# Kernel optimization log

Measured on AMD Instinct MI355X. Metric: run time of the kernel, lower is better.

## Reference

```python
import jax, jax.numpy as jnp
import numpy as np

UNITS = 64
CHANNEL = 64
L1 = 32
L2 = 32
BATCH = 64


def setup_inputs() -> dict:
    key = jax.random.key(0)
    k1, k2, k3, k4, k5 = jax.random.split(key, 5)
    input_dim = CHANNEL + 3 * UNITS
    inputs = jax.random.normal(k1, (BATCH, CHANNEL, L1, L2), dtype=jnp.float32)
    W = jax.random.normal(k2, (input_dim, UNITS * 7), dtype=jnp.float32) * (1.0 / np.sqrt(input_dim))
    U_rec = jax.random.normal(k3, (UNITS * 3, UNITS), dtype=jnp.float32) * (1.0 / np.sqrt(UNITS * 3))
    bias = jnp.zeros((UNITS * 8,), dtype=jnp.float32)
    W_ij = jax.random.normal(k4, (CHANNEL, UNITS), dtype=jnp.float32) * (1.0 / np.sqrt(CHANNEL))
    return {"inputs": inputs, "W": W, "U_rec": U_rec, "bias": bias, "W_ij": W_ij}


def reference(inputs, W, U_rec, bias, W_ij):
    B, C, l1, l2 = inputs.shape
    u = W_ij.shape[1]
    wr, br = W[:, : 3 * u], bias[: 3 * u]
    wz, bz = W[:, 3 * u : 7 * u], bias[3 * u : 7 * u]
    b_ij = bias[7 * u :]

    # [L1*L2, B, C] scan order: row-major over (i, j), direction 'lt'
    x = jnp.transpose(inputs, (2, 3, 0, 1)).reshape(l1 * l2, B, C)
    states0 = jnp.zeros((l1 + 1, l2 + 1, B, u), dtype=inputs.dtype)  # zero boundary

    def step(carry, xs):
        states, _ = carry
        s_ij, t = xs
        i = t // l2
        j = t % l2
        h_diag = states[i, j]        # [B, u]
        h_top = states[i, j + 1]
        h_left = states[i + 1, j]
        # q = [h_top, h_left, h_diag, s_ij] : [B, 3u + C]
        q = jnp.concatenate([h_top, h_left, h_diag, s_ij], axis=1)
        r = jax.nn.sigmoid(q @ wr + br)                     # [B, 3u]
        z = q @ wz + bz                                     # [B, 4u]
        zg = jax.nn.softmax(z.reshape(B, 4, u), axis=1)     # softmax across 4 gates per unit
        zi, zl, zt, zd = zg[:, 0], zg[:, 1], zg[:, 2], zg[:, 3]
        h_hat = jnp.tanh(
            s_ij @ W_ij + b_ij
            + (r * jnp.concatenate([h_left, h_top, h_diag], axis=1)) @ U_rec
        )
        h_ij = zl * h_left + zt * h_top + zd * h_diag + zi * h_hat
        states = states.at[i + 1, j + 1].set(h_ij)
        return (states, h_ij), None

    tsteps = jnp.arange(l1 * l2)
    (_, h_last), _ = jax.lax.scan(
        step, (states0, jnp.zeros((B, u), dtype=inputs.dtype)), (x, tsteps)
    )
    return h_last
```

## Files before the change

### kernel.cpp

```cpp
#include <hip/hip_runtime.h>
#include <cstdint>
#include <cstddef>


#define LDIM   32
#define BATCH  64
#define UNITS  64
#define CHAN   64
#define NBT    4
#define BT     16
#define TPB    512

typedef _Float16 f16;
typedef _Float16 f16x8 __attribute__((ext_vector_type(8)));
typedef float    f32x4 __attribute__((ext_vector_type(4)));

__global__ __launch_bounds__(TPB, 2) void spatial_gru_kernel(
    const float* __restrict__ x,
    const float* __restrict__ W,
    const float* __restrict__ Urec,
    const float* __restrict__ bias,
    const float* __restrict__ Wij,
    float* __restrict__ out,
    uint32_t* __restrict__ hbuf)
{
    const int bid = blockIdx.x;
    const int row = bid >> 2;
    const int bt  = bid & 3;
    const int b0  = bt * BT;
    const int t   = (int)threadIdx.x;
    const int u   = t & 63;
    const int g   = t >> 6;
    const int l15 = t & 15;
    const int lq  = (t & 63) >> 4;

    __shared__ __attribute__((aligned(16))) f16 qf[BT][264];
    __shared__ __attribute__((aligned(16))) f16 rf[BT][200];
    __shared__ float qs32[BT][204];
    __shared__ float Gsz [BT][260];
    __shared__ float pacc[4][BT][68];

    f16x8 wreg[4][8];
    float bias1[4] = {0.f, 0.f, 0.f, 0.f};
    if (g < 7) {
        const int nb = g * 64 + l15;
#pragma unroll
        for (int T = 0; T < 4; ++T) {
            bias1[T] = bias[nb + 16 * T];
#pragma unroll
            for (int s = 0; s < 8; ++s) {
                f16x8 v;
#pragma unroll
                for (int jj = 0; jj < 8; ++jj) {
                    int kk = s * 32 + lq * 8 + jj;
                    v[jj] = (f16)W[(size_t)kk * 448 + nb + 16 * T];
                }
                wreg[T][s] = v;
            }
        }
    }
    f16x8 wreg2[4][2];
    {
        const int kb = (g & 3) * 64;
#pragma unroll
        for (int T = 0; T < 4; ++T) {
            const int nn = T * 16 + l15;
#pragma unroll
            for (int s = 0; s < 2; ++s) {
                f16x8 v;
#pragma unroll
                for (int jj = 0; jj < 8; ++jj) {
                    int kk = kb + s * 32 + lq * 8 + jj;
                    float wv = (kk < 192) ? Urec[kk * 64 + nn] : Wij[(kk - 192) * 64 + nn];
                    v[jj] = (f16)wv;
                }
                wreg2[T][s] = v;
            }
        }
    }
    const float bij = bias[448 + u];

    for (int idx = t; idx < 192 * BT; idx += TPB) {
        int b = idx & 15, k = idx >> 4;
        qs32[b][k] = 0.f;
        qf[b][k] = (f16)0.f;
    }

    const size_t xb0 = (size_t)(b0 + g) * 65536 + (size_t)u * 1024 + (size_t)row * 32;
    const size_t xb1 = xb0 + (size_t)8 * 65536;
    {
        float x0 = x[xb0], x1 = x[xb1];
        qf[g][192 + u]     = (f16)x0;
        qf[g + 8][192 + u] = (f16)x1;
    }
    __syncthreads();

    for (int j = 0; j < LDIM; ++j) {
        float ht0 = 0.f, ht1 = 0.f;
        f16 hf0 = (f16)0.f, hf1 = (f16)0.f;
        if (row > 0) {
            const uint32_t* sp =
                hbuf + ((((size_t)(row - 1) * LDIM + j) * NBT + bt) << 9) + (g << 6) + u;
            uint32_t w = __hip_atomic_load(sp, __ATOMIC_RELAXED, __HIP_MEMORY_SCOPE_AGENT);
            while ((w & 0x00010001u) != 0x00010001u) {
                __builtin_amdgcn_s_sleep(1);
                w = __hip_atomic_load(sp, __ATOMIC_RELAXED, __HIP_MEMORY_SCOPE_AGENT);
            }
            uint16_t lo = (uint16_t)(w & 0xFFFFu), hi = (uint16_t)(w >> 16);
            hf0 = __builtin_bit_cast(f16, lo);
            hf1 = __builtin_bit_cast(f16, hi);
            ht0 = (float)hf0;
            ht1 = (float)hf1;
        }
        qs32[g][u]     = ht0;  qf[g][u]     = hf0;
        qs32[g + 8][u] = ht1;  qf[g + 8][u] = hf1;
        __syncthreads();

        float nx0 = 0.f, nx1 = 0.f;
        if (j < LDIM - 1) { nx0 = x[xb0 + j + 1]; nx1 = x[xb1 + j + 1]; }

        if (g < 7) {
            f32x4 acc[4];
#pragma unroll
            for (int T = 0; T < 4; ++T)
                acc[T] = (f32x4){bias1[T], bias1[T], bias1[T], bias1[T]};
#pragma unroll
            for (int s = 0; s < 8; ++s) {
                f16x8 a = *(const f16x8*)&qf[l15][s * 32 + lq * 8];
#pragma unroll
                for (int T = 0; T < 4; ++T)
                    acc[T] = __builtin_amdgcn_mfma_f32_16x16x32_f16(a, wreg[T][s], acc[T], 0, 0, 0);
            }
            if (g < 3) {
                const int colbase = (g == 0) ? 64 : (g == 1) ? 0 : 128;
#pragma unroll
                for (int T = 0; T < 4; ++T)
#pragma unroll
                    for (int r = 0; r < 4; ++r) {
                        float rr = 1.f / (1.f + __expf(-acc[T][r]));
                        int b = lq * 4 + r;
                        float hv = qs32[b][colbase + T * 16 + l15];
                        rf[b][g * 64 + T * 16 + l15] = (f16)(rr * hv);
                    }
            } else {
                const int zb = (g - 3) * 64;
#pragma unroll
                for (int T = 0; T < 4; ++T)
#pragma unroll
                    for (int r = 0; r < 4; ++r)
                        Gsz[lq * 4 + r][zb + T * 16 + l15] = acc[T][r];
            }
        } else {
            f32x4 a2[4];
#pragma unroll
            for (int T = 0; T < 4; ++T) a2[T] = (f32x4){0.f, 0.f, 0.f, 0.f};
#pragma unroll
            for (int s = 0; s < 2; ++s) {
                f16x8 a = *(const f16x8*)&qf[l15][192 + s * 32 + lq * 8];
#pragma unroll
                for (int T = 0; T < 4; ++T)
                    a2[T] = __builtin_amdgcn_mfma_f32_16x16x32_f16(a, wreg2[T][s], a2[T], 0, 0, 0);
            }
#pragma unroll
            for (int T = 0; T < 4; ++T)
#pragma unroll
                for (int r = 0; r < 4; ++r)
                    pacc[3][lq * 4 + r][T * 16 + l15] = a2[T][r];
        }
        __syncthreads();

        if (g >= 4 && g < 7) {
            const int w  = g - 4;
            const int kb = w * 64;
            f32x4 a2[4];
#pragma unroll
            for (int T = 0; T < 4; ++T) a2[T] = (f32x4){0.f, 0.f, 0.f, 0.f};
#pragma unroll
            for (int s = 0; s < 2; ++s) {
                f16x8 a = *(const f16x8*)&rf[l15][kb + s * 32 + lq * 8];
#pragma unroll
                for (int T = 0; T < 4; ++T)
                    a2[T] = __builtin_amdgcn_mfma_f32_16x16x32_f16(a, wreg2[T][s], a2[T], 0, 0, 0);
            }
#pragma unroll
            for (int T = 0; T < 4; ++T)
#pragma unroll
                for (int r = 0; r < 4; ++r)
                    pacc[w][lq * 4 + r][T * 16 + l15] = a2[T][r];
        }
        __syncthreads();

        float hvv[2], hTv[2];
#pragma unroll
        for (int i = 0; i < 2; ++i) {
            int b = g + 8 * i;
            float hhv = bij + pacc[0][b][u] + pacc[1][b][u] + pacc[2][b][u] + pacc[3][b][u];
            float e2 = __expf(2.f * hhv);
            float th = 1.f - 2.f / (e2 + 1.f);
            float zi = Gsz[b][u],       zl = Gsz[b][64 + u];
            float zt = Gsz[b][128 + u], zd = Gsz[b][192 + u];
            float mx = fmaxf(fmaxf(zi, zl), fmaxf(zt, zd));
            float ei = __expf(zi - mx), el = __expf(zl - mx);
            float et = __expf(zt - mx), ed = __expf(zd - mx);
            float inv = 1.f / (ei + el + et + ed);
            float hT = qs32[b][u], hL = qs32[b][64 + u], hD = qs32[b][128 + u];
            float hv = (el * hL + et * hT + ed * hD + ei * th) * inv;
            hvv[i] = hv; hTv[i] = hT;
        }
        {
            uint16_t lo = (uint16_t)(__builtin_bit_cast(uint16_t, (f16)hvv[0]) | 1u);
            uint16_t hi = (uint16_t)(__builtin_bit_cast(uint16_t, (f16)hvv[1]) | 1u);
            uint32_t pw = ((uint32_t)hi << 16) | lo;
            __hip_atomic_store(
                hbuf + ((((size_t)row * LDIM + j) * NBT + bt) << 9) + (g << 6) + u,
                pw, __ATOMIC_RELAXED, __HIP_MEMORY_SCOPE_AGENT);
        }
        if (row == LDIM - 1 && j == LDIM - 1) {
            out[(size_t)(b0 + g) * UNITS + u]     = hvv[0];
            out[(size_t)(b0 + g + 8) * UNITS + u] = hvv[1];
        }
#pragma unroll
        for (int i = 0; i < 2; ++i) {
            int b = g + 8 * i;
            qs32[b][128 + u] = hTv[i];
            qs32[b][64 + u]  = hvv[i];
            f16 htf = qf[b][u];
            qf[b][128 + u] = htf;
            qf[b][64 + u]  = (f16)hvv[i];
        }
        qf[g][192 + u]     = (f16)nx0;
        qf[g + 8][192 + u] = (f16)nx1;
    }
}

extern "C" void kernel_launch(void* const* d_in, const int* in_sizes, int n_in,
                              void* d_out, int out_size, void* d_ws, size_t ws_size,
                              hipStream_t stream) {
    const float* x    = (const float*)d_in[0];
    const float* W    = (const float*)d_in[1];
    const float* Urec = (const float*)d_in[2];
    const float* bias = (const float*)d_in[3];
    const float* Wij  = (const float*)d_in[4];
    float* out = (float*)d_out;

    uint32_t* hbuf = (uint32_t*)d_ws;

    spatial_gru_kernel<<<LDIM * NBT, TPB, 0, stream>>>(
        x, W, Urec, bias, Wij, out, hbuf);
}
```

Baseline: 264.8 us.

## Overlap cross-block h_top wait with local MFMAs and restructure the gate epilogue

After: 358.4 us. 35.3% more time.

```diff
diff --git a/kernel.cpp b/kernel.cpp
--- a/kernel.cpp
+++ b/kernel.cpp
@@ -14,6 +14,7 @@
 typedef _Float16 f16;
 typedef _Float16 f16x8 __attribute__((ext_vector_type(8)));
 typedef float    f32x4 __attribute__((ext_vector_type(4)));
+typedef uint32_t u32x4 __attribute__((ext_vector_type(4)));
 
 __global__ __launch_bounds__(TPB, 2) void spatial_gru_kernel(
     const float* __restrict__ x,
@@ -60,7 +61,7 @@
         }
     }
     f16x8 wreg2[4][2];
-    {
+    if (g >= 4) {
         const int kb = (g & 3) * 64;
 #pragma unroll
         for (int T = 0; T < 4; ++T) {
@@ -80,8 +81,8 @@
     }
     const float bij = bias[448 + u];
 
-    for (int idx = t; idx < 192 * BT; idx += TPB) {
-        int b = idx & 15, k = idx >> 4;
+    for (int idx = t; idx < 128 * BT; idx += TPB) {
+        int b = idx & 15, k = 64 + (idx >> 4);
         qs32[b][k] = 0.f;
         qf[b][k] = (f16)0.f;
     }
@@ -93,54 +94,90 @@
         qf[g][192 + u]     = (f16)x0;
         qf[g + 8][192 + u] = (f16)x1;
     }
-    __syncthreads();
 
     for (int j = 0; j < LDIM; ++j) {
-        float ht0 = 0.f, ht1 = 0.f;
-        f16 hf0 = (f16)0.f, hf1 = (f16)0.f;
+        __syncthreads();
+
+        uint32_t d0=0,d1=0,d2=0,d3=0,d4=0,d5=0,d6=0,d7=0;
+        const uint32_t* sp = hbuf;
         if (row > 0) {
-            const uint32_t* sp =
-                hbuf + ((((size_t)(row - 1) * LDIM + j) * NBT + bt) << 9) + (g << 6) + u;
-            uint32_t w = __hip_atomic_load(sp, __ATOMIC_RELAXED, __HIP_MEMORY_SCOPE_AGENT);
-            while ((w & 0x00010001u) != 0x00010001u) {
-                __builtin_amdgcn_s_sleep(1);
-                w = __hip_atomic_load(sp, __ATOMIC_RELAXED, __HIP_MEMORY_SCOPE_AGENT);
-            }
-            uint16_t lo = (uint16_t)(w & 0xFFFFu), hi = (uint16_t)(w >> 16);
-            hf0 = __builtin_bit_cast(f16, lo);
-            hf1 = __builtin_bit_cast(f16, hi);
-            ht0 = (float)hf0;
-            ht1 = (float)hf1;
-        }
-        qs32[g][u]     = ht0;  qf[g][u]     = hf0;
-        qs32[g + 8][u] = ht1;  qf[g + 8][u] = hf1;
-        __syncthreads();
-
+            sp = hbuf + ((((size_t)(row - 1) * LDIM + j) * NBT + bt) << 9)
+                      + (l15 * 32 + lq * 4);
+            d0 = __hip_atomic_load(sp + 0,  __ATOMIC_RELAXED, __HIP_MEMORY_SCOPE_AGENT);
+            d1 = __hip_atomic_load(sp + 1,  __ATOMIC_RELAXED, __HIP_MEMORY_SCOPE_AGENT);
+            d2 = __hip_atomic_load(sp + 2,  __ATOMIC_RELAXED, __HIP_MEMORY_SCOPE_AGENT);
+            d3 = __hip_atomic_load(sp + 3,  __ATOMIC_RELAXED, __HIP_MEMORY_SCOPE_AGENT);
+            d4 = __hip_atomic_load(sp + 16, __ATOMIC_RELAXED, __HIP_MEMORY_SCOPE_AGENT);
+            d5 = __hip_atomic_load(sp + 17, __ATOMIC_RELAXED, __HIP_MEMORY_SCOPE_AGENT);
+            d6 = __hip_atomic_load(sp + 18, __ATOMIC_RELAXED, __HIP_MEMORY_SCOPE_AGENT);
+            d7 = __hip_atomic_load(sp + 19, __ATOMIC_RELAXED, __HIP_MEMORY_SCOPE_AGENT);
+        }
         float nx0 = 0.f, nx1 = 0.f;
         if (j < LDIM - 1) { nx0 = x[xb0 + j + 1]; nx1 = x[xb1 + j + 1]; }
 
+        f32x4 acc[4];
         if (g < 7) {
-            f32x4 acc[4];
 #pragma unroll
             for (int T = 0; T < 4; ++T)
                 acc[T] = (f32x4){bias1[T], bias1[T], bias1[T], bias1[T]};
 #pragma unroll
-            for (int s = 0; s < 8; ++s) {
+            for (int s = 2; s < 8; ++s) {
                 f16x8 a = *(const f16x8*)&qf[l15][s * 32 + lq * 8];
 #pragma unroll
                 for (int T = 0; T < 4; ++T)
                     acc[T] = __builtin_amdgcn_mfma_f32_16x16x32_f16(a, wreg[T][s], acc[T], 0, 0, 0);
             }
+        } else {
+            f32x4 a2[4];
+#pragma unroll
+            for (int T = 0; T < 4; ++T) a2[T] = (f32x4){0.f, 0.f, 0.f, 0.f};
+#pragma unroll
+            for (int s = 0; s < 2; ++s) {
+                f16x8 a = *(const f16x8*)&qf[l15][192 + s * 32 + lq * 8];
+#pragma unroll
+                for (int T = 0; T < 4; ++T)
+                    a2[T] = __builtin_amdgcn_mfma_f32_16x16x32_f16(a, wreg2[T][s], a2[T], 0, 0, 0);
+            }
+#pragma unroll
+            for (int T = 0; T < 4; ++T)
+#pragma unroll
+                for (int r = 0; r < 4; ++r)
+                    pacc[3][lq * 4 + r][T * 16 + l15] = a2[T][r];
+        }
+
+        f16x8 ha0, ha1;
+#pragma unroll
+        for (int jj = 0; jj < 8; ++jj) { ha0[jj] = (f16)0.f; ha1[jj] = (f16)0.f; }
+        if (row > 0) {
+            while (((d0 & d1 & d2 & d3 & d4 & d5 & d6 & d7) & 0x00010001u) != 0x00010001u) {
+                __builtin_amdgcn_s_sleep(1);
+                d0 = __hip_atomic_load(sp + 0,  __ATOMIC_RELAXED, __HIP_MEMORY_SCOPE_AGENT);
+                d1 = __hip_atomic_load(sp + 1,  __ATOMIC_RELAXED, __HIP_MEMORY_SCOPE_AGENT);
+                d2 = __hip_atomic_load(sp + 2,  __ATOMIC_RELAXED, __HIP_MEMORY_SCOPE_AGENT);
+                d3 = __hip_atomic_load(sp + 3,  __ATOMIC_RELAXED, __HIP_MEMORY_SCOPE_AGENT);
+                d4 = __hip_atomic_load(sp + 16, __ATOMIC_RELAXED, __HIP_MEMORY_SCOPE_AGENT);
+                d5 = __hip_atomic_load(sp + 17, __ATOMIC_RELAXED, __HIP_MEMORY_SCOPE_AGENT);
+                d6 = __hip_atomic_load(sp + 18, __ATOMIC_RELAXED, __HIP_MEMORY_SCOPE_AGENT);
+                d7 = __hip_atomic_load(sp + 19, __ATOMIC_RELAXED, __HIP_MEMORY_SCOPE_AGENT);
+            }
+            ha0 = __builtin_bit_cast(f16x8, (u32x4){d0, d1, d2, d3});
+            ha1 = __builtin_bit_cast(f16x8, (u32x4){d4, d5, d6, d7});
+        }
+
+        if (g < 7) {
+#pragma unroll
+            for (int T = 0; T < 4; ++T)
+                acc[T] = __builtin_amdgcn_mfma_f32_16x16x32_f16(ha0, wreg[T][0], acc[T], 0, 0, 0);
+#pragma unroll
+            for (int T = 0; T < 4; ++T)
+                acc[T] = __builtin_amdgcn_mfma_f32_16x16x32_f16(ha1, wreg[T][1], acc[T], 0, 0, 0);
             if (g < 3) {
-                const int colbase = (g == 0) ? 64 : (g == 1) ? 0 : 128;
 #pragma unroll
                 for (int T = 0; T < 4; ++T)
 #pragma unroll
                     for (int r = 0; r < 4; ++r) {
                         float rr = 1.f / (1.f + __expf(-acc[T][r]));
-                        int b = lq * 4 + r;
-                        float hv = qs32[b][colbase + T * 16 + l15];
-                        rf[b][g * 64 + T * 16 + l15] = (f16)(rr * hv);
+                        rf[lq * 4 + r][g * 64 + T * 16 + l15] = (f16)rr;
                     }
             } else {
                 const int zb = (g - 3) * 64;
@@ -151,33 +188,29 @@
                         Gsz[lq * 4 + r][zb + T * 16 + l15] = acc[T][r];
             }
         } else {
-            f32x4 a2[4];
-#pragma unroll
-            for (int T = 0; T < 4; ++T) a2[T] = (f32x4){0.f, 0.f, 0.f, 0.f};
-#pragma unroll
-            for (int s = 0; s < 2; ++s) {
-                f16x8 a = *(const f16x8*)&qf[l15][192 + s * 32 + lq * 8];
-#pragma unroll
-                for (int T = 0; T < 4; ++T)
-                    a2[T] = __builtin_amdgcn_mfma_f32_16x16x32_f16(a, wreg2[T][s], a2[T], 0, 0, 0);
-            }
-#pragma unroll
-            for (int T = 0; T < 4; ++T)
-#pragma unroll
-                for (int r = 0; r < 4; ++r)
-                    pacc[3][lq * 4 + r][T * 16 + l15] = a2[T][r];
+#pragma unroll
+            for (int jj = 0; jj < 8; ++jj) {
+                qs32[l15][lq * 8 + jj]      = (float)ha0[jj];
+                qs32[l15][32 + lq * 8 + jj] = (float)ha1[jj];
+            }
         }
         __syncthreads();
 
         if (g >= 4 && g < 7) {
             const int w  = g - 4;
             const int kb = w * 64;
+            const int hb = (w == 0) ? 64 : (w == 1) ? 0 : 128;
             f32x4 a2[4];
 #pragma unroll
             for (int T = 0; T < 4; ++T) a2[T] = (f32x4){0.f, 0.f, 0.f, 0.f};
 #pragma unroll
             for (int s = 0; s < 2; ++s) {
-                f16x8 a = *(const f16x8*)&rf[l15][kb + s * 32 + lq * 8];
+                f16x8 a;
+#pragma unroll
+                for (int jj = 0; jj < 8; ++jj) {
+                    int kk = s * 32 + lq * 8 + jj;
+                    a[jj] = (f16)((float)rf[l15][kb + kk] * qs32[l15][hb + kk]);
+                }
 #pragma unroll
                 for (int T = 0; T < 4; ++T)
                     a2[T] = __builtin_amdgcn_mfma_f32_16x16x32_f16(a, wreg2[T][s], a2[T], 0, 0, 0);
@@ -187,33 +220,39 @@
 #pragma unroll
                 for (int r = 0; r < 4; ++r)
                     pacc[w][lq * 4 + r][T * 16 + l15] = a2[T][r];
+        } else if (g < 4) {
+#pragma unroll
+            for (int i = 0; i < 4; ++i) {
+                const int b = g * 4 + i;
+                float zi = Gsz[b][u],       zl = Gsz[b][64 + u];
+                float zt = Gsz[b][128 + u], zd = Gsz[b][192 + u];
+                float hT = qs32[b][u], hL = qs32[b][64 + u], hD = qs32[b][128 + u];
+                float mx = fmaxf(fmaxf(zi, zl), fmaxf(zt, zd));
+                float ei = __expf(zi - mx), el = __expf(zl - mx);
+                float et = __expf(zt - mx), ed = __expf(zd - mx);
+                float inv = 1.f / (ei + el + et + ed);
+                Gsz[b][u]      = (el * hL + et * hT + ed * hD) * inv;
+                Gsz[b][64 + u] = ei * inv;
+            }
         }
         __syncthreads();
 
         float hvv[2], hTv[2];
 #pragma unroll
         for (int i = 0; i < 2; ++i) {
-            int b = g + 8 * i;
-            float hhv = bij + pacc[0][b][u] + pacc[1][b][u] + pacc[2][b][u] + pacc[3][b][u];
-            float e2 = __expf(2.f * hhv);
+            const int b = g + 8 * i;
+            float hh = bij + pacc[0][b][u] + pacc[1][b][u] + pacc[2][b][u] + pacc[3][b][u];
+            float e2 = __expf(2.f * hh);
             float th = 1.f - 2.f / (e2 + 1.f);
-            float zi = Gsz[b][u],       zl = Gsz[b][64 + u];
-            float zt = Gsz[b][128 + u], zd = Gsz[b][192 + u];
-            float mx = fmaxf(fmaxf(zi, zl), fmaxf(zt, zd));
-            float ei = __expf(zi - mx), el = __expf(zl - mx);
-            float et = __expf(zt - mx), ed = __expf(zd - mx);
-            float inv = 1.f / (ei + el + et + ed);
-            float hT = qs32[b][u], hL = qs32[b][64 + u], hD = qs32[b][128 + u];
-            float hv = (el * hL + et * hT + ed * hD + ei * th) * inv;
-            hvv[i] = hv; hTv[i] = hT;
+            hvv[i] = Gsz[b][u] + Gsz[b][64 + u] * th;
+            hTv[i] = qs32[b][u];
         }
         {
-            uint16_t lo = (uint16_t)(__builtin_bit_cast(uint16_t, (f16)hvv[0]) | 1u);
-            uint16_t hi = (uint16_t)(__builtin_bit_cast(uint16_t, (f16)hvv[1]) | 1u);
-            uint32_t pw = ((uint32_t)hi << 16) | lo;
-            __hip_atomic_store(
-                hbuf + ((((size_t)row * LDIM + j) * NBT + bt) << 9) + (g << 6) + u,
-                pw, __ATOMIC_RELAXED, __HIP_MEMORY_SCOPE_AGENT);
+            uint16_t* hp = (uint16_t*)(hbuf + ((((size_t)row * LDIM + j) * NBT + bt) << 9));
+            uint16_t v0 = (uint16_t)(__builtin_bit_cast(uint16_t, (f16)hvv[0]) | 1u);
+            uint16_t v1 = (uint16_t)(__builtin_bit_cast(uint16_t, (f16)hvv[1]) | 1u);
+            __hip_atomic_store(hp + (g * 64 + u),       v0, __ATOMIC_RELAXED, __HIP_MEMORY_SCOPE_AGENT);
+            __hip_atomic_store(hp + ((g + 8) * 64 + u), v1, __ATOMIC_RELAXED, __HIP_MEMORY_SCOPE_AGENT);
         }
         if (row == LDIM - 1 && j == LDIM - 1) {
             out[(size_t)(b0 + g) * UNITS + u]     = hvv[0];
@@ -221,11 +260,10 @@
         }
 #pragma unroll
         for (int i = 0; i < 2; ++i) {
-            int b = g + 8 * i;
+            const int b = g + 8 * i;
             qs32[b][128 + u] = hTv[i];
             qs32[b][64 + u]  = hvv[i];
-            f16 htf = qf[b][u];
-            qf[b][128 + u] = htf;
+            qf[b][128 + u] = (f16)hTv[i];
             qf[b][64 + u]  = (f16)hvv[i];
         }
         qf[g][192 + u]     = (f16)nx0;
```

## Overlap top-state wait with non-dependent MFMAs and precompute softmax gates early

Applied to the files above, without the earlier changes.

Result: faster. 259.4 us (-2.1%).

```diff
diff --git a/kernel.cpp b/kernel.cpp
--- a/kernel.cpp
+++ b/kernel.cpp
@@ -24,15 +24,17 @@
     float* __restrict__ out,
     uint32_t* __restrict__ hbuf)
 {
-    const int bid = blockIdx.x;
-    const int row = bid >> 2;
-    const int bt  = bid & 3;
-    const int b0  = bt * BT;
-    const int t   = (int)threadIdx.x;
-    const int u   = t & 63;
-    const int g   = t >> 6;
-    const int l15 = t & 15;
-    const int lq  = (t & 63) >> 4;
+    const int p    = blockIdx.x;
+    const int xcd  = p & 7;
+    const int slot = p >> 3;
+    const int row  = xcd * 4 + (slot >> 2);
+    const int bt   = slot & 3;
+    const int b0   = bt * BT;
+    const int t    = (int)threadIdx.x;
+    const int u    = t & 63;
+    const int g    = t >> 6;
+    const int l15  = t & 15;
+    const int lq   = (t & 63) >> 4;
 
     __shared__ __attribute__((aligned(16))) f16 qf[BT][264];
     __shared__ __attribute__((aligned(16))) f16 rf[BT][200];
@@ -93,43 +95,78 @@
         qf[g][192 + u]     = (f16)x0;
         qf[g + 8][192 + u] = (f16)x1;
     }
-    __syncthreads();
 
     for (int j = 0; j < LDIM; ++j) {
-        float ht0 = 0.f, ht1 = 0.f;
-        f16 hf0 = (f16)0.f, hf1 = (f16)0.f;
+        __syncthreads();
+
+        uint32_t w = 0;
+        const uint32_t* sp = hbuf;
         if (row > 0) {
-            const uint32_t* sp =
-                hbuf + ((((size_t)(row - 1) * LDIM + j) * NBT + bt) << 9) + (g << 6) + u;
-            uint32_t w = __hip_atomic_load(sp, __ATOMIC_RELAXED, __HIP_MEMORY_SCOPE_AGENT);
-            while ((w & 0x00010001u) != 0x00010001u) {
-                __builtin_amdgcn_s_sleep(1);
-                w = __hip_atomic_load(sp, __ATOMIC_RELAXED, __HIP_MEMORY_SCOPE_AGENT);
-            }
-            uint16_t lo = (uint16_t)(w & 0xFFFFu), hi = (uint16_t)(w >> 16);
-            hf0 = __builtin_bit_cast(f16, lo);
-            hf1 = __builtin_bit_cast(f16, hi);
-            ht0 = (float)hf0;
-            ht1 = (float)hf1;
-        }
-        qs32[g][u]     = ht0;  qf[g][u]     = hf0;
-        qs32[g + 8][u] = ht1;  qf[g + 8][u] = hf1;
-        __syncthreads();
-
+            sp = hbuf + ((((size_t)(row - 1) * LDIM + j) * NBT + bt) << 9) + (g << 6) + u;
+            w = __hip_atomic_load(sp, __ATOMIC_RELAXED, __HIP_MEMORY_SCOPE_AGENT);
+        }
         float nx0 = 0.f, nx1 = 0.f;
         if (j < LDIM - 1) { nx0 = x[xb0 + j + 1]; nx1 = x[xb1 + j + 1]; }
 
+        f32x4 acc[4];
         if (g < 7) {
-            f32x4 acc[4];
 #pragma unroll
             for (int T = 0; T < 4; ++T)
                 acc[T] = (f32x4){bias1[T], bias1[T], bias1[T], bias1[T]};
 #pragma unroll
-            for (int s = 0; s < 8; ++s) {
+            for (int s = 2; s < 8; ++s) {
                 f16x8 a = *(const f16x8*)&qf[l15][s * 32 + lq * 8];
 #pragma unroll
                 for (int T = 0; T < 4; ++T)
                     acc[T] = __builtin_amdgcn_mfma_f32_16x16x32_f16(a, wreg[T][s], acc[T], 0, 0, 0);
+            }
+        } else {
+            f32x4 a2[4];
+#pragma unroll
+            for (int T = 0; T < 4; ++T) a2[T] = (f32x4){0.f, 0.f, 0.f, 0.f};
+#pragma unroll
+            for (int s = 0; s < 2; ++s) {
+                f16x8 a = *(const f16x8*)&qf[l15][192 + s * 32 + lq * 8];
+#pragma unroll
+                for (int T = 0; T < 4; ++T)
+                    a2[T] = __builtin_amdgcn_mfma_f32_16x16x32_f16(a, wreg2[T][s], a2[T], 0, 0, 0);
+            }
+#pragma unroll
+            for (int T = 0; T < 4; ++T)
+#pragma unroll
+                for (int r = 0; r < 4; ++r)
+                    pacc[3][lq * 4 + r][T * 16 + l15] = a2[T][r];
+        }
+
+        {
+            float ht0 = 0.f, ht1 = 0.f;
+            f16 hf0 = (f16)0.f, hf1 = (f16)0.f;
+            if (row > 0) {
+                while ((w & 0x00010001u) != 0x00010001u) {
+                    __builtin_amdgcn_s_sleep(1);
+                    w = __hip_atomic_load(sp, __ATOMIC_RELAXED, __HIP_MEMORY_SCOPE_AGENT);
+                }
+                uint16_t lo = (uint16_t)(w & 0xFFFFu), hi = (uint16_t)(w >> 16);
+                hf0 = __builtin_bit_cast(f16, lo);
+                hf1 = __builtin_bit_cast(f16, hi);
+                ht0 = (float)hf0;
+                ht1 = (float)hf1;
+            }
+            qs32[g][u]     = ht0;  qf[g][u]     = hf0;
+            qs32[g + 8][u] = ht1;  qf[g + 8][u] = hf1;
+        }
+        __syncthreads();
+
+        if (g < 7) {
+            {
+                f16x8 a0 = *(const f16x8*)&qf[l15][lq * 8];
+                f16x8 a1 = *(const f16x8*)&qf[l15][32 + lq * 8];
+#pragma unroll
+                for (int T = 0; T < 4; ++T)
+                    acc[T] = __builtin_amdgcn_mfma_f32_16x16x32_f16(a0, wreg[T][0], acc[T], 0, 0, 0);
+#pragma unroll
+                for (int T = 0; T < 4; ++T)
+                    acc[T] = __builtin_amdgcn_mfma_f32_16x16x32_f16(a1, wreg[T][1], acc[T], 0, 0, 0);
             }
             if (g < 3) {
                 const int colbase = (g == 0) ? 64 : (g == 1) ? 0 : 128;
@@ -150,28 +187,12 @@
                     for (int r = 0; r < 4; ++r)
                         Gsz[lq * 4 + r][zb + T * 16 + l15] = acc[T][r];
             }
-        } else {
-            f32x4 a2[4];
-#pragma unroll
-            for (int T = 0; T < 4; ++T) a2[T] = (f32x4){0.f, 0.f, 0.f, 0.f};
-#pragma unroll
-            for (int s = 0; s < 2; ++s) {
-                f16x8 a = *(const f16x8*)&qf[l15][192 + s * 32 + lq * 8];
-#pragma unroll
-                for (int T = 0; T < 4; ++T)
-                    a2[T] = __builtin_amdgcn_mfma_f32_16x16x32_f16(a, wreg2[T][s], a2[T], 0, 0, 0);
-            }
-#pragma unroll
-            for (int T = 0; T < 4; ++T)
-#pragma unroll
-                for (int r = 0; r < 4; ++r)
-                    pacc[3][lq * 4 + r][T * 16 + l15] = a2[T][r];
         }
         __syncthreads();
 
         if (g >= 4 && g < 7) {
-            const int w  = g - 4;
-            const int kb = w * 64;
+            const int wv = g - 4;
+            const int kb = wv * 64;
             f32x4 a2[4];
 #pragma unroll
             for (int T = 0; T < 4; ++T) a2[T] = (f32x4){0.f, 0.f, 0.f, 0.f};
@@ -186,26 +207,33 @@
             for (int T = 0; T < 4; ++T)
 #pragma unroll
                 for (int r = 0; r < 4; ++r)
-                    pacc[w][lq * 4 + r][T * 16 + l15] = a2[T][r];
+                    pacc[wv][lq * 4 + r][T * 16 + l15] = a2[T][r];
+        } else if (g < 4) {
+#pragma unroll
+            for (int i = 0; i < 4; ++i) {
+                const int b = g * 4 + i;
+                float zi = Gsz[b][u],       zl = Gsz[b][64 + u];
+                float zt = Gsz[b][128 + u], zd = Gsz[b][192 + u];
+                float hT = qs32[b][u], hL = qs32[b][64 + u], hD = qs32[b][128 + u];
+                float mx = fmaxf(fmaxf(zi, zl), fmaxf(zt, zd));
+                float ei = __expf(zi - mx), el = __expf(zl - mx);
+                float et = __expf(zt - mx), ed = __expf(zd - mx);
+                float inv = 1.f / (ei + el + et + ed);
+                Gsz[b][u]      = (el * hL + et * hT + ed * hD) * inv;
+                Gsz[b][64 + u] = ei * inv;
+            }
         }
         __syncthreads();
 
         float hvv[2], hTv[2];
 #pragma unroll
         for (int i = 0; i < 2; ++i) {
-            int b = g + 8 * i;
-            float hhv = bij + pacc[0][b][u] + pacc[1][b][u] + pacc[2][b][u] + pacc[3][b][u];
-            float e2 = __expf(2.f * hhv);
+            const int b = g + 8 * i;
+            float hh = bij + pacc[0][b][u] + pacc[1][b][u] + pacc[2][b][u] + pacc[3][b][u];
+            float e2 = __expf(2.f * hh);
             float th = 1.f - 2.f / (e2 + 1.f);
-            float zi = Gsz[b][u],       zl = Gsz[b][64 + u];
-            float zt = Gsz[b][128 + u], zd = Gsz[b][192 + u];
-            float mx = fmaxf(fmaxf(zi, zl), fmaxf(zt, zd));
-            float ei = __expf(zi - mx), el = __expf(zl - mx);
-            float et = __expf(zt - mx), ed = __expf(zd - mx);
-            float inv = 1.f / (ei + el + et + ed);
-            float hT = qs32[b][u], hL = qs32[b][64 + u], hD = qs32[b][128 + u];
-            float hv = (el * hL + et * hT + ed * hD + ei * th) * inv;
-            hvv[i] = hv; hTv[i] = hT;
+            hvv[i] = Gsz[b][u] + Gsz[b][64 + u] * th;
+            hTv[i] = qs32[b][u];
         }
         {
             uint16_t lo = (uint16_t)(__builtin_bit_cast(uint16_t, (f16)hvv[0]) | 1u);
@@ -221,11 +249,10 @@
         }
 #pragma unroll
         for (int i = 0; i < 2; ++i) {
-            int b = g + 8 * i;
+            const int b = g + 8 * i;
             qs32[b][128 + u] = hTv[i];
             qs32[b][64 + u]  = hvv[i];
-            f16 htf = qf[b][u];
-            qf[b][128 + u] = htf;
+            qf[b][128 + u] = (f16)hTv[i];
             qf[b][64 + u]  = (f16)hvv[i];
         }
         qf[g][192 + u]     = (f16)nx0;
```
